# Optimization experiments

Measured on AMD Instinct MI355X. Metric: run time of the kernel, lower is better.

## Reference

```python
import jax, jax.numpy as jnp
import numpy as np

NUM_HEADS = 12
EPS = 1e-12  # torch F.normalize clamp_min eps


def _l2norm(t):
    return t / jnp.clip(jnp.linalg.norm(t, axis=-1, keepdims=True), EPS)


def setup_inputs() -> dict:
    key = jax.random.key(0)
    ks = jax.random.split(key, 6)
    B, N, C = 8, 4096, 768
    Nc, Nb, F = 1, 512, 16
    s = 0.02
    return {
        "x": jax.random.normal(ks[0], (B, N, C), jnp.float32),
        "bank": jax.random.normal(ks[1], (Nc, Nb, F), jnp.float32),
        "Wq": jax.random.normal(ks[2], (C, C), jnp.float32) * s,
        "Wkv": jax.random.normal(ks[3], (F, 2 * C), jnp.float32) * s,
        "Wlin": jax.random.normal(ks[4], (C, C), jnp.float32) * s,
        "b_lin": jnp.zeros((C,), jnp.float32),
        "prelu_a": jnp.asarray(0.25, jnp.float32),
        "temperature": jnp.ones((NUM_HEADS, 1, 1), jnp.float32),
    }


def reference(x, bank, Wq, Wkv, Wlin, b_lin, prelu_a, temperature):
    B, N, C = x.shape
    Nc, Nb, _ = bank.shape
    H = NUM_HEADS
    d = C // H
    # q: (B, H, N, d), L2-normalized along d
    q = _l2norm((x @ Wq).reshape(B, N, H, d).transpose(0, 2, 1, 3))
    # kv from (detached) bank: (2, Nc, H, Nb, d)
    kv = (bank @ Wkv).reshape(Nc, Nb, 2, H, d).transpose(2, 0, 3, 1, 4)
    k = _l2norm(kv[0])
    v = kv[1]
    # cosine attention with per-head learned temperature: (B, Nc, H, N, Nb)
    attn = jnp.einsum('bhnd,chmd->bchnm', q, k) * temperature
    attn = jax.nn.softmax(attn, axis=-1)
    # (dropout is identity in eval mode)
    out = jnp.einsum('bchnm,chmd->bchnd', attn, v)  # (B, Nc, H, N, d)
    out = out.reshape(B * Nc, H, N, d).transpose(0, 2, 1, 3).reshape(B, N, C)
    out = out @ Wlin + b_lin
    # PReLU with a single shared parameter
    return jnp.where(out >= 0, out, prelu_a * out)
```

## Files before the change

kernel.cpp:

```cpp
#include <hip/hip_runtime.h>
#include <cstdint>
#include <cstddef>

typedef unsigned short u16;
typedef __attribute__((ext_vector_type(8))) __bf16 bf16x8;
typedef __attribute__((ext_vector_type(4))) float f32x4;

#define MFMA(a, b, c) __builtin_amdgcn_mfma_f32_16x16x32_bf16(a, b, c, 0, 0, 0)

__device__ __forceinline__ u16 f2bf(float f) {
  union { float f; uint32_t u; } x; x.f = f;
  uint32_t r = x.u + 0x7fffu + ((x.u >> 16) & 1u);
  return (u16)(r >> 16);
}

__device__ __forceinline__ void gld16(const u16* g, u16* l) {
  __builtin_amdgcn_global_load_lds(
      (const __attribute__((address_space(1))) void*)g,
      (__attribute__((address_space(3))) void*)l, 16, 0, 0);
}

__global__ void cvt_f32_bf16(const float* __restrict__ src, u16* __restrict__ dst, int n4) {
  int i = blockIdx.x * blockDim.x + threadIdx.x;
  int stride = gridDim.x * blockDim.x;
  for (; i < n4; i += stride) {
    float4 v = ((const float4*)src)[i];
    ushort4 o;
    o.x = f2bf(v.x); o.y = f2bf(v.y); o.z = f2bf(v.z); o.w = f2bf(v.w);
    ((ushort4*)dst)[i] = o;
  }
}

__global__ void transpose_cvt2(const float* __restrict__ s0, u16* __restrict__ d0,
                               const float* __restrict__ s1, u16* __restrict__ d1,
                               int R, int C) {
  const float* src = blockIdx.z ? s1 : s0;
  u16* dst = blockIdx.z ? d1 : d0;
  __shared__ float tile[32][33];
  int bx = blockIdx.x * 32, by = blockIdx.y * 32;
  int tx = threadIdx.x, ty = threadIdx.y;
  #pragma unroll
  for (int i = ty; i < 32; i += 8)
    tile[i][tx] = src[(size_t)(by + i) * C + bx + tx];
  __syncthreads();
  #pragma unroll
  for (int i = ty; i < 32; i += 8)
    dst[(size_t)(bx + i) * R + by + tx] = f2bf(tile[tx][i]);
}

__global__ void kv_prep(const float* __restrict__ bank, const float* __restrict__ Wkv,
                        const float* __restrict__ temp, u16* __restrict__ K, u16* __restrict__ VT) {
  int m = blockIdx.x & 511, h = blockIdx.x >> 9;
  int j = threadIdx.x;
  const float* br = bank + m * 16;
  float kj = 0.f, vj = 0.f;
  #pragma unroll
  for (int f = 0; f < 16; ++f) {
    float bv = br[f];
    kj = fmaf(bv, Wkv[f * 1536 + h * 64 + j], kj);
    vj = fmaf(bv, Wkv[f * 1536 + 768 + h * 64 + j], vj);
  }
  float ss = kj * kj;
  #pragma unroll
  for (int o = 32; o; o >>= 1) ss += __shfl_xor(ss, o);
  float rn = rsqrtf(fmaxf(ss, 1e-24f));
  K[((size_t)h * 512 + m) * 64 + j] = f2bf(kj * rn * temp[h] * 1.4426950408889634f);
  VT[((size_t)h * 64 + j) * 512 + m] = f2bf(vj);
}

template <int MODE>
__global__ __launch_bounds__(256, 3) void gemm_bt(
    const u16* __restrict__ A, const u16* __restrict__ BT, void* __restrict__ Cout,
    int M, int N, int K, const float* __restrict__ bias, const float* __restrict__ prelu) {
  __shared__ u16 sA[3][128 * 32];
  __shared__ u16 sB[3][128 * 32];
  const int ntiles = N >> 7;
  const int swz = (blockIdx.x & 7) * (gridDim.x >> 3) + (blockIdx.x >> 3);
  const int m0 = (swz / ntiles) << 7;
  const int n0 = (swz % ntiles) << 7;
  const int tid = threadIdx.x;
  const int w = tid >> 6, lane = tid & 63;
  const int wm = (w >> 1) << 6, wn = (w & 1) << 6;
  const int srow = lane >> 2, scol = (lane & 3) << 3;
  const u16* ga = A + (size_t)(m0 + (w << 5) + srow) * K + scol;
  const u16* gb = BT + (size_t)(n0 + (w << 5) + srow) * K + scol;
  const int lofs = (w << 5) * 32;
  const int fr = lane & 15, fq = (lane >> 4) << 3;
  f32x4 acc[4][4] = {};

  auto stage = [&](int buf, int k0) {
    gld16(ga + k0, sA[buf] + lofs);
    gld16(ga + k0 + (size_t)16 * K, sA[buf] + lofs + 16 * 32);
    gld16(gb + k0, sB[buf] + lofs);
    gld16(gb + k0 + (size_t)16 * K, sB[buf] + lofs + 16 * 32);
  };

  const int nk = K >> 5;
  stage(0, 0);
  stage(1, 32);
  int cb = 0;
  int sb = 2;
  for (int it = 0; it < nk; ++it) {
    asm volatile("s_waitcnt vmcnt(4)\n\ts_barrier" ::: "memory");
    int nx = it + 2; if (nx >= nk) nx -= nk;
    stage(sb, nx << 5);
    bf16x8 af[4], bfr[4];
    #pragma unroll
    for (int t = 0; t < 4; ++t) {
      af[t] = *(const bf16x8*)(sA[cb] + (wm + t * 16 + fr) * 32 + fq);
      bfr[t] = *(const bf16x8*)(sB[cb] + (wn + t * 16 + fr) * 32 + fq);
    }
    #pragma unroll
    for (int i = 0; i < 4; ++i)
      #pragma unroll
      for (int j = 0; j < 4; ++j)
        acc[i][j] = MFMA(af[i], bfr[j], acc[i][j]);
    cb = (cb == 2) ? 0 : cb + 1;
    sb = (sb == 2) ? 0 : sb + 1;
  }

  const int q = lane >> 4;
  float a = (MODE == 1) ? prelu[0] : 0.f;
  #pragma unroll
  for (int tm = 0; tm < 4; ++tm)
    #pragma unroll
    for (int tn = 0; tn < 4; ++tn) {
      int col = n0 + wn + tn * 16 + fr;
      float bv = (MODE == 1) ? bias[col] : 0.f;
      #pragma unroll
      for (int r = 0; r < 4; ++r) {
        int row = m0 + wm + tm * 16 + q * 4 + r;
        float v = acc[tm][tn][r];
        if (MODE == 1) {
          v += bv;
          v = v >= 0.f ? v : v * a;
          ((float*)Cout)[(size_t)row * N + col] = v;
        } else {
          ((u16*)Cout)[(size_t)row * N + col] = f2bf(v);
        }
      }
    }
}

__global__ __launch_bounds__(512, 4) void attn_kern(
    const u16* __restrict__ Q, const u16* __restrict__ Kb,
    const u16* __restrict__ Vt, u16* __restrict__ O) {
  __shared__ __align__(16) u16 sK[2][64 * 72];
  __shared__ __align__(16) u16 sV[2][64 * 72];

  const int qb = blockIdx.x & 127;
  const int h = blockIdx.x >> 7;
  const int tid = threadIdx.x, w = tid >> 6, lane = tid & 63;
  const int fr = lane & 15, quad = lane >> 4;
  const int rowbase = qb * 256 + (w << 5);

  bf16x8 qa[2][2];
  #pragma unroll
  for (int g = 0; g < 2; ++g) {
    const u16* qp = Q + (size_t)(rowbase + g * 16 + fr) * 768 + h * 64 + (quad << 3);
    qa[g][0] = *(const bf16x8*)qp;
    qa[g][1] = *(const bf16x8*)(qp + 32);
    float ss = 0.f;
    #pragma unroll
    for (int j = 0; j < 8; ++j) {
      float f0 = (float)qa[g][0][j], f1 = (float)qa[g][1][j];
      ss += f0 * f0 + f1 * f1;
    }
    ss += __shfl_xor(ss, 16);
    ss += __shfl_xor(ss, 32);
    float rn = rsqrtf(fmaxf(ss, 1e-24f));
    #pragma unroll
    for (int j = 0; j < 8; ++j) {
      qa[g][0][j] = (__bf16)((float)qa[g][0][j] * rn);
      qa[g][1][j] = (__bf16)((float)qa[g][1][j] * rn);
    }
  }

  const u16* kg = Kb + (size_t)h * 512 * 64;
  const u16* vg = Vt + (size_t)h * 64 * 512;
  int4 kreg, vreg;
  auto load_chunk = [&](int c) {
    kreg = *(const int4*)(kg + (size_t)(c * 64 + (tid >> 3)) * 64 + (tid & 7) * 8);
    vreg = *(const int4*)(vg + (size_t)(tid >> 3) * 512 + c * 64 + (tid & 7) * 8);
  };
  auto store_chunk = [&](int buf) {
    *(int4*)(sK[buf] + (tid >> 3) * 72 + (tid & 7) * 8) = kreg;
    *(int4*)(sV[buf] + (tid >> 3) * 72 + (tid & 7) * 8) = vreg;
  };

  load_chunk(0);
  store_chunk(0);
  load_chunk(1);
  __syncthreads();

  f32x4 oa[2][4] = {};
  float ls[2] = {0.f, 0.f};

  for (int c = 0; c < 8; ++c) {
    const int cb = c & 1;
    if (c < 7) store_chunk((c + 1) & 1);
    if (c < 6) load_chunk(c + 2);

    #pragma unroll
    for (int ks = 0; ks < 2; ++ks) {
      f32x4 s[2][2];
      #pragma unroll
      for (int half = 0; half < 2; ++half) {
        const int mt = ks * 2 + half;
        const u16* kp = sK[cb] + (mt * 16 + fr) * 72 + (quad << 3);
        bf16x8 ak0 = *(const bf16x8*)kp;
        bf16x8 ak1 = *(const bf16x8*)(kp + 32);
        #pragma unroll
        for (int g = 0; g < 2; ++g) {
          f32x4 z = {0.f, 0.f, 0.f, 0.f};
          z = MFMA(ak0, qa[g][0], z);
          z = MFMA(ak1, qa[g][1], z);
          s[g][half] = z;
        }
      }
      bf16x8 pbf[2];
      #pragma unroll
      for (int g = 0; g < 2; ++g)
        #pragma unroll
        for (int half = 0; half < 2; ++half)
          #pragma unroll
          for (int r = 0; r < 4; ++r) {
            float p = __builtin_amdgcn_exp2f(s[g][half][r]);
            ls[g] += p;
            pbf[g][half * 4 + r] = (__bf16)p;
          }
      #pragma unroll
      for (int t = 0; t < 4; ++t) {
        const u16* vp = sV[cb] + (t * 16 + fr) * 72 + ks * 32 + (quad << 2);
        bf16x8 va;
        *(uint2*)&va = *(const uint2*)vp;
        *((uint2*)&va + 1) = *(const uint2*)(vp + 16);
        #pragma unroll
        for (int g = 0; g < 2; ++g)
          oa[g][t] = MFMA(va, pbf[g], oa[g][t]);
      }
    }
    __syncthreads();
  }

  #pragma unroll
  for (int g = 0; g < 2; ++g) {
    float l = ls[g];
    l += __shfl_xor(l, 16);
    l += __shfl_xor(l, 32);
    float rl = __builtin_amdgcn_rcpf(l);
    u16* op = O + (size_t)(rowbase + g * 16 + fr) * 768 + h * 64 + (quad << 2);
    #pragma unroll
    for (int t = 0; t < 4; ++t) {
      ushort4 pk;
      pk.x = f2bf(oa[g][t][0] * rl);
      pk.y = f2bf(oa[g][t][1] * rl);
      pk.z = f2bf(oa[g][t][2] * rl);
      pk.w = f2bf(oa[g][t][3] * rl);
      *(ushort4*)(op + t * 16) = pk;
    }
  }
}

extern "C" void kernel_launch(void* const* d_in, const int* in_sizes, int n_in,
                              void* d_out, int out_size, void* d_ws, size_t ws_size,
                              hipStream_t stream) {
  const float* x      = (const float*)d_in[0];
  const float* bank   = (const float*)d_in[1];
  const float* Wq     = (const float*)d_in[2];
  const float* Wkv    = (const float*)d_in[3];
  const float* Wlin   = (const float*)d_in[4];
  const float* b_lin  = (const float*)d_in[5];
  const float* prelu  = (const float*)d_in[6];
  const float* temp   = (const float*)d_in[7];
  float* out = (float*)d_out;

  char* ws = (char*)d_ws;
  const size_t NELEM = 25165824;
  u16* qbuf  = (u16*)ws;
  u16* xbuf  = (u16*)(ws + 50331648);
  u16* obuf  = xbuf;
  u16* wqt   = (u16*)(ws + 100663296);
  u16* wlt   = wqt + 589824;
  u16* kbuf  = wlt + 589824;
  u16* vtbuf = kbuf + 393216;

  cvt_f32_bf16<<<4096, 256, 0, stream>>>(x, xbuf, (int)(NELEM / 4));
  transpose_cvt2<<<dim3(24, 24, 2), dim3(32, 8), 0, stream>>>(Wq, wqt, Wlin, wlt, 768, 768);
  kv_prep<<<6144, 64, 0, stream>>>(bank, Wkv, temp, kbuf, vtbuf);
  gemm_bt<0><<<1536, 256, 0, stream>>>(xbuf, wqt, qbuf, 32768, 768, 768, nullptr, nullptr);
  attn_kern<<<1536, 512, 0, stream>>>(qbuf, kbuf, vtbuf, obuf);
  gemm_bt<1><<<1536, 256, 0, stream>>>(obuf, wlt, out, 32768, 768, 768, b_lin, prelu);
}
```

Baseline: 359.0 us.

## Fuse x fp32-to-bf16 conversion into Q GEMM load path and merge prep kernels

The standalone pass converting x (8x4096x768 fp32) to bf16 is removed. The Q projection GEMM now streams fp32 tiles of x directly into LDS with an XOR swizzle and converts them to bf16 while building MFMA fragments. This avoids writing and re-reading a 50MB bf16 intermediate. The weight transpose and K/V prep kernels are merged into one launch to cut launch overhead. In exchange the first GEMM doubles its A-tile LDS footprint and occupancy drops to 2 blocks per CU, and the fp32 A loads move twice the bytes per tile.

New measurement: 391.5 us. 9.1% more time.

```diff
diff --git a/kernel.cpp b/kernel.cpp
--- a/kernel.cpp
+++ b/kernel.cpp
@@ -14,65 +14,59 @@
   return (u16)(r >> 16);
 }
 
-__device__ __forceinline__ void gld16(const u16* g, u16* l) {
+__device__ __forceinline__ void gld16(const void* g, u16* l) {
   __builtin_amdgcn_global_load_lds(
       (const __attribute__((address_space(1))) void*)g,
       (__attribute__((address_space(3))) void*)l, 16, 0, 0);
 }
 
-__global__ void cvt_f32_bf16(const float* __restrict__ src, u16* __restrict__ dst, int n4) {
-  int i = blockIdx.x * blockDim.x + threadIdx.x;
-  int stride = gridDim.x * blockDim.x;
-  for (; i < n4; i += stride) {
-    float4 v = ((const float4*)src)[i];
-    ushort4 o;
-    o.x = f2bf(v.x); o.y = f2bf(v.y); o.z = f2bf(v.z); o.w = f2bf(v.w);
-    ((ushort4*)dst)[i] = o;
-  }
-}
-
-__global__ void transpose_cvt2(const float* __restrict__ s0, u16* __restrict__ d0,
-                               const float* __restrict__ s1, u16* __restrict__ d1,
-                               int R, int C) {
-  const float* src = blockIdx.z ? s1 : s0;
-  u16* dst = blockIdx.z ? d1 : d0;
-  __shared__ float tile[32][33];
-  int bx = blockIdx.x * 32, by = blockIdx.y * 32;
-  int tx = threadIdx.x, ty = threadIdx.y;
-  #pragma unroll
-  for (int i = ty; i < 32; i += 8)
-    tile[i][tx] = src[(size_t)(by + i) * C + bx + tx];
-  __syncthreads();
-  #pragma unroll
-  for (int i = ty; i < 32; i += 8)
-    dst[(size_t)(bx + i) * R + by + tx] = f2bf(tile[tx][i]);
-}
-
-__global__ void kv_prep(const float* __restrict__ bank, const float* __restrict__ Wkv,
-                        const float* __restrict__ temp, u16* __restrict__ K, u16* __restrict__ VT) {
-  int m = blockIdx.x & 511, h = blockIdx.x >> 9;
-  int j = threadIdx.x;
-  const float* br = bank + m * 16;
-  float kj = 0.f, vj = 0.f;
-  #pragma unroll
-  for (int f = 0; f < 16; ++f) {
-    float bv = br[f];
-    kj = fmaf(bv, Wkv[f * 1536 + h * 64 + j], kj);
-    vj = fmaf(bv, Wkv[f * 1536 + 768 + h * 64 + j], vj);
-  }
-  float ss = kj * kj;
-  #pragma unroll
-  for (int o = 32; o; o >>= 1) ss += __shfl_xor(ss, o);
-  float rn = rsqrtf(fmaxf(ss, 1e-24f));
-  K[((size_t)h * 512 + m) * 64 + j] = f2bf(kj * rn * temp[h] * 1.4426950408889634f);
-  VT[((size_t)h * 64 + j) * 512 + m] = f2bf(vj);
+__global__ void prep_kern(const float* __restrict__ Wq, u16* __restrict__ wqt,
+                          const float* __restrict__ Wlin, u16* __restrict__ wlt,
+                          const float* __restrict__ bank, const float* __restrict__ Wkv,
+                          const float* __restrict__ temp, u16* __restrict__ Kb,
+                          u16* __restrict__ VT) {
+  const int b = blockIdx.x;
+  if (b < 1152) {
+    __shared__ float tile[32][33];
+    const float* src = (b >= 576) ? Wlin : Wq;
+    u16* dst = (b >= 576) ? wlt : wqt;
+    const int r = (b >= 576) ? b - 576 : b;
+    const int bx = (r % 24) * 32, by = (r / 24) * 32;
+    const int tx = threadIdx.x & 31, ty = threadIdx.x >> 5;
+    #pragma unroll
+    for (int i = ty; i < 32; i += 8)
+      tile[i][tx] = src[(size_t)(by + i) * 768 + bx + tx];
+    __syncthreads();
+    #pragma unroll
+    for (int i = ty; i < 32; i += 8)
+      dst[(size_t)(bx + i) * 768 + by + tx] = f2bf(tile[tx][i]);
+  } else {
+    const int bb = b - 1152;
+    const int h = bb >> 7;
+    const int m = ((bb & 127) << 2) + (threadIdx.x >> 6);
+    const int j = threadIdx.x & 63;
+    const float* br = bank + m * 16;
+    float kj = 0.f, vj = 0.f;
+    #pragma unroll
+    for (int f = 0; f < 16; ++f) {
+      float bv = br[f];
+      kj = fmaf(bv, Wkv[f * 1536 + h * 64 + j], kj);
+      vj = fmaf(bv, Wkv[f * 1536 + 768 + h * 64 + j], vj);
+    }
+    float ss = kj * kj;
+    #pragma unroll
+    for (int o = 32; o; o >>= 1) ss += __shfl_xor(ss, o);
+    float rn = rsqrtf(fmaxf(ss, 1e-24f));
+    Kb[((size_t)h * 512 + m) * 64 + j] = f2bf(kj * rn * temp[h] * 1.4426950408889634f);
+    VT[((size_t)h * 64 + j) * 512 + m] = f2bf(vj);
+  }
 }
 
 template <int MODE>
-__global__ __launch_bounds__(256, 3) void gemm_bt(
-    const u16* __restrict__ A, const u16* __restrict__ BT, void* __restrict__ Cout,
+__global__ __launch_bounds__(256, MODE ? 3 : 2) void gemm_bt(
+    const void* __restrict__ Ain, const u16* __restrict__ BT, void* __restrict__ Cout,
     int M, int N, int K, const float* __restrict__ bias, const float* __restrict__ prelu) {
-  __shared__ u16 sA[3][128 * 32];
+  __shared__ u16 sA[3][MODE ? 128 * 32 : 128 * 64];
   __shared__ u16 sB[3][128 * 32];
   const int ntiles = N >> 7;
   const int swz = (blockIdx.x & 7) * (gridDim.x >> 3) + (blockIdx.x >> 3);
@@ -82,15 +76,23 @@
   const int w = tid >> 6, lane = tid & 63;
   const int wm = (w >> 1) << 6, wn = (w & 1) << 6;
   const int srow = lane >> 2, scol = (lane & 3) << 3;
-  const u16* ga = A + (size_t)(m0 + (w << 5) + srow) * K + scol;
   const u16* gb = BT + (size_t)(n0 + (w << 5) + srow) * K + scol;
   const int lofs = (w << 5) * 32;
   const int fr = lane & 15, fq = (lane >> 4) << 3;
+  const u16* ga16 = (const u16*)Ain + (size_t)(m0 + (w << 5) + srow) * K + scol;
+  const float* gaf = (const float*)Ain + (size_t)(m0 + (w << 5) + (lane >> 3)) * K
+                     + (((lane & 7) ^ (lane >> 3)) << 2);
   f32x4 acc[4][4] = {};
 
   auto stage = [&](int buf, int k0) {
-    gld16(ga + k0, sA[buf] + lofs);
-    gld16(ga + k0 + (size_t)16 * K, sA[buf] + lofs + 16 * 32);
+    if (MODE) {
+      gld16(ga16 + k0, sA[buf] + lofs);
+      gld16(ga16 + k0 + (size_t)16 * K, sA[buf] + lofs + 16 * 32);
+    } else {
+      #pragma unroll
+      for (int r = 0; r < 4; ++r)
+        gld16(gaf + k0 + (size_t)(r << 3) * K, sA[buf] + (w << 11) + (r << 9));
+    }
     gld16(gb + k0, sB[buf] + lofs);
     gld16(gb + k0 + (size_t)16 * K, sB[buf] + lofs + 16 * 32);
   };
@@ -101,13 +103,25 @@
   int cb = 0;
   int sb = 2;
   for (int it = 0; it < nk; ++it) {
-    asm volatile("s_waitcnt vmcnt(4)\n\ts_barrier" ::: "memory");
+    if (MODE) asm volatile("s_waitcnt vmcnt(4)\n\ts_barrier" ::: "memory");
+    else      asm volatile("s_waitcnt vmcnt(6)\n\ts_barrier" ::: "memory");
     int nx = it + 2; if (nx >= nk) nx -= nk;
     stage(sb, nx << 5);
     bf16x8 af[4], bfr[4];
     #pragma unroll
     for (int t = 0; t < 4; ++t) {
-      af[t] = *(const bf16x8*)(sA[cb] + (wm + t * 16 + fr) * 32 + fq);
+      if (MODE) {
+        af[t] = *(const bf16x8*)(sA[cb] + (wm + t * 16 + fr) * 32 + fq);
+      } else {
+        const float* sAf = (const float*)sA[cb];
+        const int c0 = fq ^ ((fr & 7) << 2);
+        f32x4 a0 = *(const f32x4*)(sAf + (wm + t * 16 + fr) * 32 + c0);
+        f32x4 a1 = *(const f32x4*)(sAf + (wm + t * 16 + fr) * 32 + (c0 ^ 4));
+        bf16x8 v;
+        #pragma unroll
+        for (int j = 0; j < 4; ++j) { v[j] = (__bf16)a0[j]; v[j + 4] = (__bf16)a1[j]; }
+        af[t] = v;
+      }
       bfr[t] = *(const bf16x8*)(sB[cb] + (wn + t * 16 + fr) * 32 + fq);
     }
     #pragma unroll
@@ -276,19 +290,15 @@
   float* out = (float*)d_out;
 
   char* ws = (char*)d_ws;
-  const size_t NELEM = 25165824;
   u16* qbuf  = (u16*)ws;
-  u16* xbuf  = (u16*)(ws + 50331648);
-  u16* obuf  = xbuf;
+  u16* obuf  = (u16*)(ws + 50331648);
   u16* wqt   = (u16*)(ws + 100663296);
   u16* wlt   = wqt + 589824;
   u16* kbuf  = wlt + 589824;
   u16* vtbuf = kbuf + 393216;
 
-  cvt_f32_bf16<<<4096, 256, 0, stream>>>(x, xbuf, (int)(NELEM / 4));
-  transpose_cvt2<<<dim3(24, 24, 2), dim3(32, 8), 0, stream>>>(Wq, wqt, Wlin, wlt, 768, 768);
-  kv_prep<<<6144, 64, 0, stream>>>(bank, Wkv, temp, kbuf, vtbuf);
-  gemm_bt<0><<<1536, 256, 0, stream>>>(xbuf, wqt, qbuf, 32768, 768, 768, nullptr, nullptr);
+  prep_kern<<<2688, 256, 0, stream>>>(Wq, wqt, Wlin, wlt, bank, Wkv, temp, kbuf, vtbuf);
+  gemm_bt<0><<<1536, 256, 0, stream>>>(x, wqt, qbuf, 32768, 768, 768, nullptr, nullptr);
   attn_kern<<<1536, 512, 0, stream>>>(qbuf, kbuf, vtbuf, obuf);
   gemm_bt<1><<<1536, 256, 0, stream>>>(obuf, wlt, out, 32768, 768, 768, b_lin, prelu);
 }
```
